# Performance work log

Measured on AMD Instinct MI355X. Metric: run time of the kernel, lower is better.

## Reference

```python
import jax, jax.numpy as jnp
import numpy as np

GRID_SIZE = 5
SPLINE_ORDER = 3
COUPLING = 0.05
LN_EPS = 1e-5
BATCH = 1024
IN_DIM = 2048
HIDDEN = [4096, 4096, 2048]


def _knots():
    k = SPLINE_ORDER
    return np.concatenate([np.full(k, -1.0), np.linspace(-1.0, 1.0, GRID_SIZE + 1), np.full(k, 1.0)])


def bspline_basis(t):
    # Replicates the module's partial in-place Cox-de Boor recursion exactly:
    # after the loops, cols[0..4] are degree-3, col 5 degree-2, col 6 degree-1, col 7 degree-0.
    knots = _knots()
    k = SPLINE_ORDER
    n = len(knots) - k - 1  # 8
    cols = [jnp.where((t >= knots[i]) & (t < knots[i + 1]), 1.0, 0.0).astype(t.dtype)
            for i in range(min(n, len(knots) - 1))]
    for degree in range(1, min(k + 1, n)):
        for i in range(n - degree):
            denom1 = knots[i + degree] - knots[i]
            denom2 = knots[i + degree + 1] - knots[i + 1]
            term1 = ((t - knots[i]) / denom1) * cols[i] if denom1 > 1e-10 else 0.0
            term2 = (((knots[i + degree + 1] - t) / denom2) * cols[i + 1]
                     if (denom2 > 1e-10 and i + 1 < n) else 0.0)
            cols[i] = term1 + term2
    return jnp.stack(cols, axis=-1)  # [..., n]


def kan_activation(x, control_points, reg_weights):
    # x: [B, D]; control_points: [D, grid+order+1]; reg_weights: [D]
    t = jnp.tanh(x)
    basis = bspline_basis(t)  # [B, D, n]
    m = min(basis.shape[-1], control_points.shape[1])  # min(8, 9) = 8
    spline = jnp.einsum('bdn,dn->bd', basis[..., :m], control_points[:, :m])
    return jnp.clip(spline * reg_weights[None, :], -10.0, 10.0)


def _generators():
    sx = np.array([[0., 1.], [1., 0.]], np.float32)
    sy = np.array([[0., -1.], [1., 0.]], np.float32)
    sz = np.array([[1., 0.], [0., -1.]], np.float32)
    return np.stack([sx, sy, sz, np.eye(2, dtype=np.float32)])  # [4,2,2]

GENS = jnp.asarray(_generators())
GEN_DIAG = jnp.asarray(np.stack([np.diagonal(g) for g in _generators()]))  # [4,2]


def noncommutative_transform(x):
    # pairs of the flattened tensor, generator index cycles mod 4
    shape = x.shape
    flat = x.reshape(-1)
    P = flat.shape[0] // 2
    vec = flat[:2 * P].reshape(P, 2)
    ng = GENS.shape[0]
    if P % ng == 0:
        v = vec.reshape(P // ng, ng, 2)                      # [Q, 4, 2]
        gv = jnp.einsum('gij,qgj->qgi', GENS, v)
        vg = v * GEN_DIAG[None, :, :]
        comm = jnp.clip(gv - vg, -1.0, 1.0)
        out = (v + COUPLING * comm).reshape(-1)
    else:
        G = GENS[jnp.arange(P) % ng]
        gv = jnp.einsum('pij,pj->pi', G, vec)
        vg = vec * jnp.diagonal(G, axis1=-2, axis2=-1)
        comm = jnp.clip(gv - vg, -1.0, 1.0)
        out = (vec + COUPLING * comm).reshape(-1)
    if flat.shape[0] % 2 == 1:
        out = jnp.concatenate([out, flat[-1:]])
    return out.reshape(shape)


def setup_inputs() -> dict:
    key = jax.random.key(0)
    ks = jax.random.split(key, 16)
    inp = {'x': jax.random.normal(ks[0], (BATCH, IN_DIM), jnp.float32)}
    prev = IN_DIM
    ncp = GRID_SIZE + SPLINE_ORDER + 1  # 9
    for li, h in enumerate(HIDDEN, start=1):
        kw, kb, kc = jax.random.split(ks[li], 3)
        inp[f'W{li}'] = jax.random.normal(kw, (h, prev), jnp.float32) / np.sqrt(prev)
        inp[f'b{li}'] = jnp.zeros((h,), jnp.float32)
        inp[f'cp{li}'] = jax.random.normal(kc, (h, ncp), jnp.float32) * 0.1
        inp[f'rw{li}'] = jnp.full((h,), 0.5, jnp.float32)
        prev = h
    inp['W_out'] = jax.random.normal(ks[10], (IN_DIM, prev), jnp.float32) / np.sqrt(prev)
    inp['b_out'] = jnp.zeros((IN_DIM,), jnp.float32)
    return inp


def reference(x, W1, b1, cp1, rw1, W2, b2, cp2, rw2, W3, b3, cp3, rw3, W_out, b_out):
    # F.layer_norm over feature dim, no affine
    mu = jnp.mean(x, axis=-1, keepdims=True)
    var = jnp.var(x, axis=-1, keepdims=True)
    cur = (x - mu) / jnp.sqrt(var + LN_EPS)
    for W, b, cp, rw in ((W1, b1, cp1, rw1), (W2, b2, cp2, rw2), (W3, b3, cp3, rw3)):
        lin = cur @ W.T + b
        kan = kan_activation(lin, cp, rw)
        cur = noncommutative_transform(kan)  # dropout = identity in eval
    return cur @ W_out.T + b_out
```

## Files before the change

kernel.cpp:

```cpp
#include <hip/hip_runtime.h>

typedef __attribute__((ext_vector_type(8))) short bf16x8;
typedef __attribute__((ext_vector_type(4))) float f32x4;

__device__ __forceinline__ float b2f(unsigned short u) {
    union { unsigned int i; float f; } x; x.i = ((unsigned int)u) << 16; return x.f;
}
__device__ __forceinline__ unsigned short f2b(float f) {
    union { float f; unsigned int i; } x; x.f = f;
    unsigned int r = x.i + 0x7fffu + ((x.i >> 16) & 1u);
    return (unsigned short)(r >> 16);
}

__device__ __forceinline__ float kan_spline(float t, const float* cpf, float rwf) {
    float c3 = (t >= -1.0f && t < -0.6f) ? 1.0f : 0.0f;
    float c4 = (t >= -0.6f && t < -0.2f) ? 1.0f : 0.0f;
    float c5 = (t >= -0.2f && t <  0.2f) ? 1.0f : 0.0f;
    float c6 = (t >=  0.2f && t <  0.6f) ? 1.0f : 0.0f;
    float c7 = (t >=  0.6f && t <  1.0f) ? 1.0f : 0.0f;
    float d2 = (-0.6f - t) * 2.5f * c3;
    float d3 = (t + 1.0f) * 2.5f * c3 + (-0.2f - t) * 2.5f * c4;
    float d4 = (t + 0.6f) * 2.5f * c4 + ( 0.2f - t) * 2.5f * c5;
    float d5 = (t + 0.2f) * 2.5f * c5 + ( 0.6f - t) * 2.5f * c6;
    float d6 = (t - 0.2f) * 2.5f * c6 + ( 1.0f - t) * 2.5f * c7;
    float e1 = (-0.6f - t) * 2.5f  * d2;
    float e2 = (t + 1.0f) * 2.5f  * d2 + (-0.2f - t) * 1.25f * d3;
    float e3 = (t + 1.0f) * 1.25f * d3 + ( 0.2f - t) * 1.25f * d4;
    float e4 = (t + 0.6f) * 1.25f * d4 + ( 0.6f - t) * 1.25f * d5;
    float e5 = (t + 0.2f) * 1.25f * d5 + ( 1.0f - t) * 1.25f * d6;
    const float r12 = 1.0f / 1.2f;
    float f0 = (-0.6f - t) * 2.5f  * e1;
    float f1 = (t + 1.0f) * 2.5f  * e1 + (-0.2f - t) * 1.25f * e2;
    float f2 = (t + 1.0f) * 1.25f * e2 + ( 0.2f - t) * r12   * e3;
    float f3 = (t + 1.0f) * r12   * e3 + ( 0.6f - t) * r12   * e4;
    float f4 = (t + 0.6f) * r12   * e4 + ( 1.0f - t) * r12   * e5;
    float sp = f0*cpf[0] + f1*cpf[1] + f2*cpf[2] + f3*cpf[3] + f4*cpf[4]
             + e5*cpf[5] + d6*cpf[6] + c7*cpf[7];
    float v = sp * rwf;
    return fminf(fmaxf(v, -10.0f), 10.0f);
}

__global__ void ln_stats_kernel(const float* __restrict__ x,
                                float* __restrict__ mu, float* __restrict__ rstd) {
    const int row = blockIdx.x;
    const float* p = x + (size_t)row * 2048 + threadIdx.x * 8;
    double s = 0.0, q = 0.0;
#pragma unroll
    for (int i = 0; i < 8; ++i) { float v = p[i]; s += v; q += (double)v * v; }
    for (int o = 32; o > 0; o >>= 1) { s += __shfl_down(s, o, 64); q += __shfl_down(q, o, 64); }
    __shared__ double shs[4], shq[4];
    const int lane = threadIdx.x & 63, w = threadIdx.x >> 6;
    if (lane == 0) { shs[w] = s; shq[w] = q; }
    __syncthreads();
    if (threadIdx.x == 0) {
        double S = shs[0] + shs[1] + shs[2] + shs[3];
        double Q = shq[0] + shq[1] + shq[2] + shq[3];
        double m = S / 2048.0;
        double var = Q / 2048.0 - m * m;
        mu[row] = (float)m;
        rstd[row] = (float)(1.0 / sqrt(var + 1e-5));
    }
}

__global__ void rowsum_kernel(const float* __restrict__ W,
                              float* __restrict__ S, int K) {
    const int lane = threadIdx.x & 63, w = threadIdx.x >> 6;
    const int row = blockIdx.x * 4 + w;
    const float* p = W + (size_t)row * K;
    double s = 0.0;
    for (int c = lane * 8; c < K; c += 512) {
#pragma unroll
        for (int i = 0; i < 8; ++i) s += p[c + i];
    }
    for (int o = 32; o > 0; o >>= 1) s += __shfl_down(s, o, 64);
    if (lane == 0) S[row] = (float)s;
}

__global__ void split2_kernel(const float* __restrict__ src,
                              unsigned short* __restrict__ dst, int C) {
    const int r = blockIdx.x;
    const int c = threadIdx.x * 8;
    const float* p = src + (size_t)r * C + c;
    float4 u0 = ((const float4*)p)[0];
    float4 u1 = ((const float4*)p)[1];
    float v[8] = {u0.x, u0.y, u0.z, u0.w, u1.x, u1.y, u1.z, u1.w};
    unsigned short hi[8], lo[8];
#pragma unroll
    for (int i = 0; i < 8; ++i) {
        hi[i] = f2b(v[i]);
        lo[i] = f2b(v[i] - b2f(hi[i]));
    }
    unsigned short* d = dst + (size_t)r * 2 * C + c;
    *(uint4*)d = *(const uint4*)hi;
    *(uint4*)(d + C) = *(const uint4*)lo;
}

__global__ void cvt_kernel(const float* __restrict__ src,
                           unsigned short* __restrict__ dst) {
    const size_t i = ((size_t)blockIdx.x * 256 + threadIdx.x) * 8;
    float4 u0 = ((const float4*)(src + i))[0];
    float4 u1 = ((const float4*)(src + i))[1];
    float v[8] = {u0.x, u0.y, u0.z, u0.w, u1.x, u1.y, u1.z, u1.w};
    unsigned short t[8];
#pragma unroll
    for (int q = 0; q < 8; ++q) t[q] = f2b(v[q]);
    *(uint4*)(dst + i) = *(const uint4*)t;
}

template <int EPI, int BSRC>
__global__ __launch_bounds__(256, 2)
void gemm_kan(const void* __restrict__ Av, const void* __restrict__ Bv,
              const float* __restrict__ bias, const float* __restrict__ cp,
              const float* __restrict__ rw, const float* __restrict__ mu,
              const float* __restrict__ rstd, const float* __restrict__ S1,
              void* __restrict__ outp,
              int Nld, int n0, int Ktot, int lda, int ldb)
{
    constexpr int BM = 64, BN = 64, BK = 64, LDP = 72;
    constexpr bool SPL = (BSRC == 2);
    constexpr int OFF_B  = BM * LDP;
    constexpr int OFF_LO = (BM + BN) * LDP;
    __shared__ unsigned short lds[(SPL ? 2 : 1) * (BM + BN) * LDP];

    const int tid  = threadIdx.x;
    const int lane = tid & 63;
    const int wid  = tid >> 6;
    const int bm = blockIdx.x * BM;
    const int bn = blockIdx.y * BN;
    const int wmo = (wid >> 1) * 32;
    const int wno = (wid & 1) * 32;
    const int fr = lane & 15;
    const int kq = lane >> 4;
    const int sar = tid >> 3, sac = (tid & 7) << 3;
    const int sfr = tid >> 2, sfc = (tid & 3) << 4;

    f32x4 acc[2][2] = {};

    uint4 pA0 = {}, pA1 = {}, pB0 = {}, pB1 = {};
    const unsigned short* Ab = (const unsigned short*)Av;
    const unsigned short* Bb = (const unsigned short*)Bv;
    const size_t a0 = (size_t)(bm + sar) * lda + sac;
    const size_t a1 = (size_t)(bm + 32 + sar) * lda + sac;
    const size_t b0 = (size_t)(bn + sar) * ldb + sac;
    const size_t b1 = (size_t)(bn + 32 + sar) * ldb + sac;
    if constexpr (BSRC == 0) {
        pA0 = *(const uint4*)(Ab + a0);
        pA1 = *(const uint4*)(Ab + a1);
        pB0 = *(const uint4*)(Bb + b0);
        pB1 = *(const uint4*)(Bb + b1);
    }

    for (int k0 = 0; k0 < Ktot; k0 += BK) {
        if constexpr (BSRC == 0) {
            *(uint4*)&lds[sar * LDP + sac] = pA0;
            *(uint4*)&lds[(32 + sar) * LDP + sac] = pA1;
            *(uint4*)&lds[OFF_B + sar * LDP + sac] = pB0;
            *(uint4*)&lds[OFF_B + (32 + sar) * LDP + sac] = pB1;
        } else {
            {
                const float* g = (const float*)Bv + (size_t)(bn + sfr) * ldb + k0 + sfc;
                float4 u0 = ((const float4*)g)[0];
                float4 u1 = ((const float4*)g)[1];
                float4 u2 = ((const float4*)g)[2];
                float4 u3 = ((const float4*)g)[3];
                float v[16] = {u0.x,u0.y,u0.z,u0.w, u1.x,u1.y,u1.z,u1.w,
                               u2.x,u2.y,u2.z,u2.w, u3.x,u3.y,u3.z,u3.w};
                unsigned short hi[16], lo[16];
#pragma unroll
                for (int i = 0; i < 16; ++i) {
                    hi[i] = f2b(v[i]);
                    if (SPL) lo[i] = f2b(v[i] - b2f(hi[i]));
                }
                unsigned short* d = &lds[OFF_B + sfr * LDP + sfc];
                ((uint4*)d)[0] = *(const uint4*)&hi[0];
                ((uint4*)d)[1] = *(const uint4*)&hi[8];
                if constexpr (SPL) {
                    unsigned short* dl = d + OFF_LO;
                    ((uint4*)dl)[0] = *(const uint4*)&lo[0];
                    ((uint4*)dl)[1] = *(const uint4*)&lo[8];
                }
            }
            if constexpr (SPL) {
                const float* g = (const float*)Av + (size_t)(bm + sfr) * lda + k0 + sfc;
                float4 u0 = ((const float4*)g)[0];
                float4 u1 = ((const float4*)g)[1];
                float4 u2 = ((const float4*)g)[2];
                float4 u3 = ((const float4*)g)[3];
                float v[16] = {u0.x,u0.y,u0.z,u0.w, u1.x,u1.y,u1.z,u1.w,
                               u2.x,u2.y,u2.z,u2.w, u3.x,u3.y,u3.z,u3.w};
                unsigned short hi[16], lo[16];
#pragma unroll
                for (int i = 0; i < 16; ++i) {
                    hi[i] = f2b(v[i]);
                    lo[i] = f2b(v[i] - b2f(hi[i]));
                }
                unsigned short* d = &lds[sfr * LDP + sfc];
                ((uint4*)d)[0] = *(const uint4*)&hi[0];
                ((uint4*)d)[1] = *(const uint4*)&hi[8];
                unsigned short* dl = d + OFF_LO;
                ((uint4*)dl)[0] = *(const uint4*)&lo[0];
                ((uint4*)dl)[1] = *(const uint4*)&lo[8];
            } else {
                *(uint4*)&lds[sar * LDP + sac] = *(const uint4*)(Ab + a0 + k0);
                *(uint4*)&lds[(32 + sar) * LDP + sac] = *(const uint4*)(Ab + a1 + k0);
            }
        }
        __syncthreads();
        if constexpr (BSRC == 0) {
            if (k0 + BK < Ktot) {
                const int kn = k0 + BK;
                const int ak = (EPI == 0) ? (kn < 4096 ? kn : kn - 4096) : kn;
                const int bk = (EPI == 0) ? (kn < 2048 ? kn : kn - 2048) : kn;
                pA0 = *(const uint4*)(Ab + a0 + ak);
                pA1 = *(const uint4*)(Ab + a1 + ak);
                pB0 = *(const uint4*)(Bb + b0 + bk);
                pB1 = *(const uint4*)(Bb + b1 + bk);
            }
        }
#pragma unroll
        for (int s = 0; s < 2; ++s) {
            const int cc = (s * 4 + kq) << 3;
            bf16x8 aF[2], bF[2];
#pragma unroll
            for (int i = 0; i < 2; ++i)
                aF[i] = *(const bf16x8*)&lds[(wmo + i * 16 + fr) * LDP + cc];
#pragma unroll
            for (int j = 0; j < 2; ++j)
                bF[j] = *(const bf16x8*)&lds[OFF_B + (wno + j * 16 + fr) * LDP + cc];
#pragma unroll
            for (int i = 0; i < 2; ++i)
#pragma unroll
                for (int j = 0; j < 2; ++j)
                    acc[i][j] = __builtin_amdgcn_mfma_f32_16x16x32_bf16(aF[i], bF[j], acc[i][j], 0, 0, 0);
            if constexpr (SPL) {
                bf16x8 aL[2], bL[2];
#pragma unroll
                for (int i = 0; i < 2; ++i)
                    aL[i] = *(const bf16x8*)&lds[OFF_LO + (wmo + i * 16 + fr) * LDP + cc];
#pragma unroll
                for (int i = 0; i < 2; ++i)
#pragma unroll
                    for (int j = 0; j < 2; ++j)
                        acc[i][j] = __builtin_amdgcn_mfma_f32_16x16x32_bf16(aL[i], bF[j], acc[i][j], 0, 0, 0);
#pragma unroll
                for (int j = 0; j < 2; ++j)
                    bL[j] = *(const bf16x8*)&lds[OFF_LO + OFF_B + (wno + j * 16 + fr) * LDP + cc];
#pragma unroll
                for (int i = 0; i < 2; ++i)
#pragma unroll
                    for (int j = 0; j < 2; ++j)
                        acc[i][j] = __builtin_amdgcn_mfma_f32_16x16x32_bf16(aF[i], bL[j], acc[i][j], 0, 0, 0);
            }
        }
        __syncthreads();
    }

    const int rowg = (lane >> 4) * 4;
#pragma unroll
    for (int j = 0; j < 2; ++j) {
        const int n = n0 + bn + wno + j * 16 + fr;
        const float bs = bias[n];
        float cpf[8], rwf = 0.0f, s1 = 0.0f;
        if (EPI < 2) {
#pragma unroll
            for (int q = 0; q < 8; ++q) cpf[q] = cp[(size_t)n * 9 + q];
            rwf = rw[n];
        }
        if (EPI == 0) s1 = S1[n];
        const int s = n & 7;
#pragma unroll
        for (int i = 0; i < 2; ++i) {
            const int m0 = bm + wmo + i * 16 + rowg;
#pragma unroll
            for (int r = 0; r < 4; ++r) {
                const int m = m0 + r;
                float v = acc[i][j][r];
                if (EPI == 0) v = (v - mu[m] * s1) * rstd[m] + bs;
                else          v += bs;
                if (EPI < 2) {
                    v = kan_spline(tanhf(v), cpf, rwf);
                    float p = __shfl_xor(v, 1, 64);
                    p = fminf(fmaxf(p, -1.0f), 1.0f);
                    if (s < 4) v += ((s == 2) ? -0.05f : 0.05f) * p;
                }
                if (EPI == 2) ((float*)outp)[(size_t)m * Nld + n] = v;
                else ((unsigned short*)outp)[(size_t)m * Nld + n] = f2b(v);
            }
        }
    }
}

extern "C" void kernel_launch(void* const* d_in, const int* in_sizes, int n_in,
                              void* d_out, int out_size, void* d_ws, size_t ws_size,
                              hipStream_t stream) {
    const float* x    = (const float*)d_in[0];
    const float* W1   = (const float*)d_in[1];
    const float* b1   = (const float*)d_in[2];
    const float* cp1  = (const float*)d_in[3];
    const float* rw1  = (const float*)d_in[4];
    const float* W2   = (const float*)d_in[5];
    const float* b2   = (const float*)d_in[6];
    const float* cp2  = (const float*)d_in[7];
    const float* rw2  = (const float*)d_in[8];
    const float* W3   = (const float*)d_in[9];
    const float* b3   = (const float*)d_in[10];
    const float* cp3  = (const float*)d_in[11];
    const float* rw3  = (const float*)d_in[12];
    const float* Wout = (const float*)d_in[13];
    const float* bout = (const float*)d_in[14];

    char* ws = (char*)d_ws;
    float* mu   = (float*)(ws);
    float* rstd = (float*)(ws + 4096);
    float* S1   = (float*)(ws + 8192);
    unsigned short* A2 = (unsigned short*)(ws + 32768);
    unsigned short* A3 = (unsigned short*)(ws + 32768 + 8388608);
    unsigned short* A4 = A2;
    unsigned short* Asplit = A3;
    unsigned short* Wb = (unsigned short*)(ws + 32768 + 2 * 8388608);
    const size_t NEED_FULL = 32768 + 2 * 8388608 + 33554432;
    const size_t NEED_HALF = 32768 + 2 * 8388608 + 16777216;

    ln_stats_kernel<<<1024, 256, 0, stream>>>(x, mu, rstd);
    rowsum_kernel<<<1024, 256, 0, stream>>>(W1, S1, 2048);

    if (ws_size >= NEED_FULL) {
        split2_kernel<<<1024, 256, 0, stream>>>(x, Asplit, 2048);
        split2_kernel<<<4096, 256, 0, stream>>>(W1, Wb, 2048);
        gemm_kan<0, 0><<<dim3(16, 64), 256, 0, stream>>>(
            Asplit, Wb, b1, cp1, rw1, mu, rstd, S1, A2, 4096, 0, 6144, 4096, 4096);
        cvt_kernel<<<8192, 256, 0, stream>>>(W2, Wb);
        gemm_kan<1, 0><<<dim3(16, 64), 256, 0, stream>>>(
            A2, Wb, b2, cp2, rw2, nullptr, nullptr, nullptr, A3, 4096, 0, 4096, 4096, 4096);
        cvt_kernel<<<4096, 256, 0, stream>>>(W3, Wb);
        gemm_kan<1, 0><<<dim3(16, 32), 256, 0, stream>>>(
            A3, Wb, b3, cp3, rw3, nullptr, nullptr, nullptr, A4, 2048, 0, 4096, 4096, 4096);
        cvt_kernel<<<2048, 256, 0, stream>>>(Wout, Wb);
        gemm_kan<2, 0><<<dim3(16, 32), 256, 0, stream>>>(
            A4, Wb, bout, nullptr, nullptr, nullptr, nullptr, nullptr, d_out, 2048, 0, 2048, 2048, 2048);
    } else if (ws_size >= NEED_HALF) {
        split2_kernel<<<1024, 256, 0, stream>>>(x, Asplit, 2048);
        for (int h = 0; h < 2; ++h) {
            split2_kernel<<<2048, 256, 0, stream>>>(W1 + (size_t)h * 2048 * 2048, Wb, 2048);
            gemm_kan<0, 0><<<dim3(16, 32), 256, 0, stream>>>(
                Asplit, Wb, b1, cp1, rw1, mu, rstd, S1, A2, 4096, h * 2048, 6144, 4096, 4096);
        }
        for (int h = 0; h < 2; ++h) {
            cvt_kernel<<<4096, 256, 0, stream>>>(W2 + (size_t)h * 2048 * 4096, Wb);
            gemm_kan<1, 0><<<dim3(16, 32), 256, 0, stream>>>(
                A2, Wb, b2, cp2, rw2, nullptr, nullptr, nullptr, A3, 4096, h * 2048, 4096, 4096, 4096);
        }
        cvt_kernel<<<4096, 256, 0, stream>>>(W3, Wb);
        gemm_kan<1, 0><<<dim3(16, 32), 256, 0, stream>>>(
            A3, Wb, b3, cp3, rw3, nullptr, nullptr, nullptr, A4, 2048, 0, 4096, 4096, 4096);
        cvt_kernel<<<2048, 256, 0, stream>>>(Wout, Wb);
        gemm_kan<2, 0><<<dim3(16, 32), 256, 0, stream>>>(
            A4, Wb, bout, nullptr, nullptr, nullptr, nullptr, nullptr, d_out, 2048, 0, 2048, 2048, 2048);
    } else {
        gemm_kan<0, 2><<<dim3(16, 64), 256, 0, stream>>>(
            x, W1, b1, cp1, rw1, mu, rstd, S1, A2, 4096, 0, 2048, 2048, 2048);
        gemm_kan<1, 1><<<dim3(16, 64), 256, 0, stream>>>(
            A2, W2, b2, cp2, rw2, nullptr, nullptr, nullptr, A3, 4096, 0, 4096, 4096, 4096);
        gemm_kan<1, 1><<<dim3(16, 32), 256, 0, stream>>>(
            A3, W3, b3, cp3, rw3, nullptr, nullptr, nullptr, A4, 2048, 0, 4096, 4096, 4096);
        gemm_kan<2, 1><<<dim3(16, 32), 256, 0, stream>>>(
            A4, Wout, bout, nullptr, nullptr, nullptr, nullptr, nullptr, d_out, 2048, 0, 2048, 2048, 2048);
    }
}
```

Measured before the change: 447.4 us.

## Add direct-to-LDS double-buffered GEMM with 64x128 tiles and grouped block swizzle

Introduces a new GEMM kernel that loads tiles straight from global memory into LDS with global_load_lds, double-buffering so the next K-slab loads while MFMAs run on the current one. It widens the N tile to 128, halves the grid, and remaps block indices in groups of 8 for better L2 reuse. The unpadded LDS layout may cause bank conflicts on fragment reads, and the larger tile reduces the number of workgroups per GEMM.

Result: no change. 449.3 us (+0.4%).

```diff
diff --git a/kernel.cpp b/kernel.cpp
--- a/kernel.cpp
+++ b/kernel.cpp
@@ -10,6 +10,11 @@
     union { float f; unsigned int i; } x; x.f = f;
     unsigned int r = x.i + 0x7fffu + ((x.i >> 16) & 1u);
     return (unsigned short)(r >> 16);
+}
+
+__device__ __forceinline__ void gl16(unsigned short* l, const unsigned short* g) {
+    __builtin_amdgcn_global_load_lds((__attribute__((address_space(1))) void*)g,
+                                     (__attribute__((address_space(3))) void*)l, 16, 0, 0);
 }
 
 __device__ __forceinline__ float kan_spline(float t, const float* cpf, float rwf) {
@@ -107,6 +112,130 @@
     *(uint4*)(dst + i) = *(const uint4*)t;
 }
 
+template <int EPI>
+__global__ __launch_bounds__(256, 2)
+void gemm_kan2(const unsigned short* __restrict__ Ab,
+               const unsigned short* __restrict__ Bb,
+               const float* __restrict__ bias, const float* __restrict__ cp,
+               const float* __restrict__ rw, const float* __restrict__ mu,
+               const float* __restrict__ rstd, const float* __restrict__ S1,
+               void* __restrict__ outp,
+               int Nld, int n0, int Ktot, int lda, int ldb)
+{
+    constexpr int BM = 64, BN = 128, BK = 64;
+    constexpr int ASZ = BM * BK;
+    constexpr int BUF = ASZ + BN * BK;
+    __shared__ unsigned short lds[2 * BUF];
+
+    const int tid  = threadIdx.x;
+    const int lane = tid & 63;
+    const int wid  = tid >> 6;
+
+    const int gx = gridDim.x;
+    int flat = blockIdx.y * gx + blockIdx.x;
+    const int nwg = gx * gridDim.y;
+    if ((nwg & 7) == 0) flat = (flat & 7) * (nwg >> 3) + (flat >> 3);
+    const int bm = (flat % gx) * BM;
+    const int bn = (flat / gx) * BN;
+
+    const int wmo = (wid >> 1) * 32;
+    const int wno = (wid & 1) * 64;
+    const int fr = lane & 15;
+    const int kq = lane >> 4;
+
+    const int uA0 = (wid << 7) + lane;
+    const int uA1 = uA0 + 64;
+    const int uB0 = (wid << 8) + lane;
+    const size_t aoff0 = (size_t)(bm + (uA0 >> 3)) * lda + ((uA0 & 7) << 3);
+    const size_t aoff1 = (size_t)(bm + (uA1 >> 3)) * lda + ((uA1 & 7) << 3);
+    const size_t boff0 = (size_t)(bn + ((uB0       ) >> 3)) * ldb + ((uB0 & 7) << 3);
+    const size_t boff1 = (size_t)(bn + ((uB0 +  64) >> 3)) * ldb + ((uB0 & 7) << 3);
+    const size_t boff2 = (size_t)(bn + ((uB0 + 128) >> 3)) * ldb + ((uB0 & 7) << 3);
+    const size_t boff3 = (size_t)(bn + ((uB0 + 192) >> 3)) * ldb + ((uB0 & 7) << 3);
+
+    f32x4 acc[2][4] = {};
+
+#define STAGE(BSEL, AK, BKK) do {                                     \
+    unsigned short* lA_ = &lds[(BSEL) * BUF];                         \
+    unsigned short* lB_ = lA_ + ASZ;                                  \
+    gl16(lA_ + uA0 * 8, Ab + aoff0 + (AK));                           \
+    gl16(lA_ + uA1 * 8, Ab + aoff1 + (AK));                           \
+    gl16(lB_ + (uB0      ) * 8, Bb + boff0 + (BKK));                  \
+    gl16(lB_ + (uB0 +  64) * 8, Bb + boff1 + (BKK));                  \
+    gl16(lB_ + (uB0 + 128) * 8, Bb + boff2 + (BKK));                  \
+    gl16(lB_ + (uB0 + 192) * 8, Bb + boff3 + (BKK));                  \
+} while (0)
+
+    STAGE(0, 0, 0);
+
+    int cur = 0;
+    for (int k0 = 0; k0 < Ktot; k0 += BK) {
+        __syncthreads();
+        if (k0 + BK < Ktot) {
+            const int kn = k0 + BK;
+            int ak = kn, bk = kn;
+            if (EPI == 0) {
+                ak = (kn < 4096) ? kn : kn - 4096;
+                bk = (kn < 2048) ? kn : kn - 2048;
+            }
+            STAGE(cur ^ 1, ak, bk);
+        }
+        const unsigned short* cl = &lds[cur * BUF];
+#pragma unroll
+        for (int s = 0; s < 2; ++s) {
+            const int cc = ((s << 2) + kq) << 3;
+            bf16x8 aF[2], bF[4];
+#pragma unroll
+            for (int i = 0; i < 2; ++i)
+                aF[i] = *(const bf16x8*)&cl[(wmo + i * 16 + fr) * BK + cc];
+#pragma unroll
+            for (int j = 0; j < 4; ++j)
+                bF[j] = *(const bf16x8*)&cl[ASZ + (wno + j * 16 + fr) * BK + cc];
+#pragma unroll
+            for (int i = 0; i < 2; ++i)
+#pragma unroll
+                for (int j = 0; j < 4; ++j)
+                    acc[i][j] = __builtin_amdgcn_mfma_f32_16x16x32_bf16(aF[i], bF[j], acc[i][j], 0, 0, 0);
+        }
+        cur ^= 1;
+    }
+#undef STAGE
+
+    const int rowg = (lane >> 4) * 4;
+#pragma unroll
+    for (int j = 0; j < 4; ++j) {
+        const int n = n0 + bn + wno + j * 16 + fr;
+        const float bs = bias[n];
+        float cpf[8], rwf = 0.0f, s1 = 0.0f;
+        if (EPI < 2) {
+#pragma unroll
+            for (int q = 0; q < 8; ++q) cpf[q] = cp[(size_t)n * 9 + q];
+            rwf = rw[n];
+        }
+        if (EPI == 0) s1 = S1[n];
+        const int s = n & 7;
+#pragma unroll
+        for (int i = 0; i < 2; ++i) {
+            const int m0 = bm + wmo + i * 16 + rowg;
+#pragma unroll
+            for (int r = 0; r < 4; ++r) {
+                const int m = m0 + r;
+                float v = acc[i][j][r];
+                if (EPI == 0) v = (v - mu[m] * s1) * rstd[m] + bs;
+                else          v += bs;
+                if (EPI < 2) {
+                    v = kan_spline(tanhf(v), cpf, rwf);
+                    float p = __shfl_xor(v, 1, 64);
+                    p = fminf(fmaxf(p, -1.0f), 1.0f);
+                    if (s < 4) v += ((s == 2) ? -0.05f : 0.05f) * p;
+                }
+                if (EPI == 2) ((float*)outp)[(size_t)m * Nld + n] = v;
+                else ((unsigned short*)outp)[(size_t)m * Nld + n] = f2b(v);
+            }
+        }
+    }
+}
+
 template <int EPI, int BSRC>
 __global__ __launch_bounds__(256, 2)
 void gemm_kan(const void* __restrict__ Av, const void* __restrict__ Bv,
@@ -327,34 +456,34 @@
     if (ws_size >= NEED_FULL) {
         split2_kernel<<<1024, 256, 0, stream>>>(x, Asplit, 2048);
         split2_kernel<<<4096, 256, 0, stream>>>(W1, Wb, 2048);
-        gemm_kan<0, 0><<<dim3(16, 64), 256, 0, stream>>>(
+        gemm_kan2<0><<<dim3(16, 32), 256, 0, stream>>>(
             Asplit, Wb, b1, cp1, rw1, mu, rstd, S1, A2, 4096, 0, 6144, 4096, 4096);
         cvt_kernel<<<8192, 256, 0, stream>>>(W2, Wb);
-        gemm_kan<1, 0><<<dim3(16, 64), 256, 0, stream>>>(
+        gemm_kan2<1><<<dim3(16, 32), 256, 0, stream>>>(
             A2, Wb, b2, cp2, rw2, nullptr, nullptr, nullptr, A3, 4096, 0, 4096, 4096, 4096);
         cvt_kernel<<<4096, 256, 0, stream>>>(W3, Wb);
-        gemm_kan<1, 0><<<dim3(16, 32), 256, 0, stream>>>(
+        gemm_kan2<1><<<dim3(16, 16), 256, 0, stream>>>(
             A3, Wb, b3, cp3, rw3, nullptr, nullptr, nullptr, A4, 2048, 0, 4096, 4096, 4096);
         cvt_kernel<<<2048, 256, 0, stream>>>(Wout, Wb);
-        gemm_kan<2, 0><<<dim3(16, 32), 256, 0, stream>>>(
+        gemm_kan2<2><<<dim3(16, 16), 256, 0, stream>>>(
             A4, Wb, bout, nullptr, nullptr, nullptr, nullptr, nullptr, d_out, 2048, 0, 2048, 2048, 2048);
     } else if (ws_size >= NEED_HALF) {
         split2_kernel<<<1024, 256, 0, stream>>>(x, Asplit, 2048);
         for (int h = 0; h < 2; ++h) {
             split2_kernel<<<2048, 256, 0, stream>>>(W1 + (size_t)h * 2048 * 2048, Wb, 2048);
-            gemm_kan<0, 0><<<dim3(16, 32), 256, 0, stream>>>(
+            gemm_kan2<0><<<dim3(16, 16), 256, 0, stream>>>(
                 Asplit, Wb, b1, cp1, rw1, mu, rstd, S1, A2, 4096, h * 2048, 6144, 4096, 4096);
         }
         for (int h = 0; h < 2; ++h) {
             cvt_kernel<<<4096, 256, 0, stream>>>(W2 + (size_t)h * 2048 * 4096, Wb);
-            gemm_kan<1, 0><<<dim3(16, 32), 256, 0, stream>>>(
+            gemm_kan2<1><<<dim3(16, 16), 256, 0, stream>>>(
                 A2, Wb, b2, cp2, rw2, nullptr, nullptr, nullptr, A3, 4096, h * 2048, 4096, 4096, 4096);
         }
         cvt_kernel<<<4096, 256, 0, stream>>>(W3, Wb);
-        gemm_kan<1, 0><<<dim3(16, 32), 256, 0, stream>>>(
+        gemm_kan2<1><<<dim3(16, 16), 256, 0, stream>>>(
             A3, Wb, b3, cp3, rw3, nullptr, nullptr, nullptr, A4, 2048, 0, 4096, 4096, 4096);
         cvt_kernel<<<2048, 256, 0, stream>>>(Wout, Wb);
-        gemm_kan<2, 0><<<dim3(16, 32), 256, 0, stream>>>(
+        gemm_kan2<2><<<dim3(16, 16), 256, 0, stream>>>(
             A4, Wb, bout, nullptr, nullptr, nullptr, nullptr, nullptr, d_out, 2048, 0, 2048, 2048, 2048);
     } else {
         gemm_kan<0, 2><<<dim3(16, 64), 256, 0, stream>>>(
```
